# Optimization experiments

Hardware: AMD Instinct MI355X
Metric: run time of the kernel (lower is better)

Reference implementation:

```python
import jax, jax.numpy as jnp
import numpy as np

IN_CH = 512
MID_CH = IN_CH // 8  # 64


def setup_inputs() -> dict:
    key = jax.random.key(0)
    ks = jax.random.split(key, 7)
    B, C, H, W = 8, IN_CH, 64, 64
    s = 1.0 / np.sqrt(C)
    x = jax.random.normal(ks[0], (B, C, H, W), dtype=jnp.float32)
    wq = jax.random.normal(ks[1], (MID_CH, C), dtype=jnp.float32) * s
    bq = jax.random.normal(ks[2], (MID_CH,), dtype=jnp.float32) * 0.01
    wk = jax.random.normal(ks[3], (MID_CH, C), dtype=jnp.float32) * s
    bk = jax.random.normal(ks[4], (MID_CH,), dtype=jnp.float32) * 0.01
    wv = jax.random.normal(ks[5], (C, C), dtype=jnp.float32) * s
    bv = jax.random.normal(ks[6], (C,), dtype=jnp.float32) * 0.01
    gamma = jnp.array([0.5], dtype=jnp.float32)
    return {"x": x, "wq": wq, "bq": bq, "wk": wk, "bk": bk,
            "wv": wv, "bv": bv, "gamma": gamma}


def reference(x, wq, bq, wk, bk, wv, bv, gamma):
    B, C, H, W = x.shape
    N = H * W
    xf = x.reshape(B, C, N)  # flatten spatial -> [B, C, N]
    # 1x1 convs are channel-wise matmuls
    q = jnp.einsum('mc,bcn->bnm', wq, xf) + bq  # [B, N, mid]
    k = jnp.einsum('mc,bcn->bmn', wk, xf) + bk[None, :, None]  # [B, mid, N]
    v = jnp.einsum('oc,bcn->bon', wv, xf) + bv[None, :, None]  # [B, C, N]
    sim = jnp.einsum('bnm,bmj->bnj', q, k)  # [B, N, N]
    sim = jax.nn.softmax(sim, axis=-1)
    # feat[b,c,i] = sum_j v[b,c,j] * sim[b,i,j]   (value @ sim^T)
    feat = jnp.einsum('bcj,bij->bci', v, sim).reshape(B, C, H, W)
    return gamma[0] * feat + x
```

## Files before the change

kernel.cpp:

```cpp
#include <hip/hip_runtime.h>
#include <hip/hip_bf16.h>


#define BB 8
#define CC 512
#define MM 64
#define NN 4096
#define LOG2E 1.4426950408889634f

typedef __attribute__((ext_vector_type(8))) short bf16x8;
typedef __attribute__((ext_vector_type(8))) _Float16 f16x8;
typedef __attribute__((ext_vector_type(4))) float f32x4;

__device__ unsigned g_kmax[BB];

__device__ __forceinline__ unsigned short f2bf(float f) {
  union { float f; unsigned u; } v; v.f = f;
  unsigned r = v.u + 0x7fffu + ((v.u >> 16) & 1u);
  return (unsigned short)(r >> 16);
}
__device__ __forceinline__ float bf2f(unsigned short h) {
  union { unsigned u; float f; } v; v.u = ((unsigned)h) << 16;
  return v.f;
}
__device__ __forceinline__ unsigned short f2h(float f) {
  union { _Float16 h; unsigned short u; } v; v.h = (_Float16)f;
  return v.u;
}

__global__ __launch_bounds__(256) void k_wconv(
    const float* __restrict__ wq, const float* __restrict__ wk,
    const float* __restrict__ wv,
    unsigned short* __restrict__ wqhi, unsigned short* __restrict__ wqlo,
    unsigned short* __restrict__ wkhi, unsigned short* __restrict__ wklo,
    unsigned short* __restrict__ wvbf) {
  const int tid = blockIdx.x * 256 + threadIdx.x;
  if (tid < BB) g_kmax[tid] = 0u;
  if (tid < MM * CC) {
    float v = wq[tid];
    unsigned short h = f2bf(v);
    wqhi[tid] = h; wqlo[tid] = f2bf(v - bf2f(h));
    v = wk[tid]; h = f2bf(v);
    wkhi[tid] = h; wklo[tid] = f2bf(v - bf2f(h));
  }
  for (int i = tid; i < CC * CC; i += 65536) wvbf[i] = f2bf(wv[i]);
}

__global__ __launch_bounds__(256) void k_transpose(const float* __restrict__ x,
                                                   unsigned short* __restrict__ xT) {
  __shared__ float tile[64][65];
  const int b = blockIdx.z, c0 = blockIdx.y * 64, n0 = blockIdx.x * 64;
  const int t = threadIdx.x;
  {
    const int nl = t & 63, cl0 = t >> 6;
    const float* xp = x + ((size_t)b * CC + c0) * NN + n0;
#pragma unroll
    for (int r = 0; r < 16; r++) {
      const int cl = cl0 + r * 4;
      tile[cl][nl] = xp[(size_t)cl * NN + nl];
    }
  }
  __syncthreads();
  {
    const int cl = t & 63, nl0 = t >> 6;
    unsigned short* xtp = xT + ((size_t)b * NN + n0) * CC + c0;
#pragma unroll
    for (int r = 0; r < 16; r++) {
      const int nl = nl0 + r * 4;
      xtp[(size_t)nl * CC + cl] = f2bf(tile[cl][nl]);
    }
  }
}

__global__ __launch_bounds__(256, 2) void k_proj(
    const unsigned short* __restrict__ xT,
    const unsigned short* __restrict__ wqhi, const unsigned short* __restrict__ wqlo,
    const unsigned short* __restrict__ wkhi, const unsigned short* __restrict__ wklo,
    const float* __restrict__ bq, const float* __restrict__ bk,
    const unsigned short* __restrict__ wvbf, const float* __restrict__ bv,
    unsigned short* __restrict__ qf, unsigned short* __restrict__ kf,
    unsigned short* __restrict__ vbf) {
  __shared__ float ksl[4][4][16];
  const int t = threadIdx.x, w = t >> 6, l = t & 63, lr = l & 15, g = l >> 4;

  if (blockIdx.x < 512) {
    const int b = blockIdx.x & 7;
    const int n0 = (blockIdx.x >> 3) * 64;
    const unsigned short* qhp = wqhi + (size_t)(w * 16 + lr) * CC + g * 8;
    const unsigned short* qlp = wqlo + (size_t)(w * 16 + lr) * CC + g * 8;
    const unsigned short* khp = wkhi + (size_t)(w * 16 + lr) * CC + g * 8;
    const unsigned short* klp = wklo + (size_t)(w * 16 + lr) * CC + g * 8;
    const unsigned short* xp = xT + ((size_t)b * NN + n0 + lr) * CC + g * 8;
    f32x4 qacc[4], kacc[4];
#pragma unroll
    for (int nf = 0; nf < 4; nf++) {
      qacc[nf] = f32x4{0.f, 0.f, 0.f, 0.f};
      kacc[nf] = f32x4{0.f, 0.f, 0.f, 0.f};
    }
    for (int cc = 0; cc < CC; cc += 32) {
      const bf16x8 qh8 = *reinterpret_cast<const bf16x8*>(qhp + cc);
      const bf16x8 ql8 = *reinterpret_cast<const bf16x8*>(qlp + cc);
      const bf16x8 kh8 = *reinterpret_cast<const bf16x8*>(khp + cc);
      const bf16x8 kl8 = *reinterpret_cast<const bf16x8*>(klp + cc);
      bf16x8 xb[4];
#pragma unroll
      for (int nf = 0; nf < 4; nf++)
        xb[nf] = *reinterpret_cast<const bf16x8*>(xp + (size_t)nf * 16 * CC + cc);
#pragma unroll
      for (int nf = 0; nf < 4; nf++) {
        qacc[nf] = __builtin_amdgcn_mfma_f32_16x16x32_bf16(qh8, xb[nf], qacc[nf], 0, 0, 0);
        qacc[nf] = __builtin_amdgcn_mfma_f32_16x16x32_bf16(ql8, xb[nf], qacc[nf], 0, 0, 0);
        kacc[nf] = __builtin_amdgcn_mfma_f32_16x16x32_bf16(kh8, xb[nf], kacc[nf], 0, 0, 0);
        kacc[nf] = __builtin_amdgcn_mfma_f32_16x16x32_bf16(kl8, xb[nf], kacc[nf], 0, 0, 0);
      }
    }
    float bqv[4], bkv[4];
#pragma unroll
    for (int r = 0; r < 4; r++) {
      bqv[r] = bq[w * 16 + g * 4 + r];
      bkv[r] = bk[w * 16 + g * 4 + r];
    }
    float kssp[4];
#pragma unroll
    for (int nf = 0; nf < 4; nf++) {
      float ks2 = 0.f;
      unsigned short qh[4], kh[4];
#pragma unroll
      for (int r = 0; r < 4; r++) {
        const float qv = (qacc[nf][r] + bqv[r]) * LOG2E;
        const float kv = kacc[nf][r] + bkv[r];
        qh[r] = f2h(qv); kh[r] = f2h(kv);
        ks2 += kv * kv;
      }
      kssp[nf] = ks2;
      const int n = n0 + nf * 16 + lr;
      const size_t base = ((size_t)b * NN + n) * MM + w * 16 + g * 4;
      *reinterpret_cast<ushort4*>(qf + base) = make_ushort4(qh[0], qh[1], qh[2], qh[3]);
      *reinterpret_cast<ushort4*>(kf + base) = make_ushort4(kh[0], kh[1], kh[2], kh[3]);
    }
#pragma unroll
    for (int nf = 0; nf < 4; nf++) {
      kssp[nf] += __shfl_xor(kssp[nf], 16);
      kssp[nf] += __shfl_xor(kssp[nf], 32);
    }
    if (l < 16) {
#pragma unroll
      for (int nf = 0; nf < 4; nf++) ksl[w][nf][lr] = kssp[nf];
    }
    __syncthreads();
    if (t < 64) {
      const int nf2 = t >> 4, lr2 = t & 15;
      float kn2 = ksl[0][nf2][lr2] + ksl[1][nf2][lr2] + ksl[2][nf2][lr2] + ksl[3][nf2][lr2];
#pragma unroll
      for (int d = 1; d < 64; d <<= 1) kn2 = fmaxf(kn2, __shfl_xor(kn2, d));
      if (t == 0) atomicMax(&g_kmax[b], __float_as_uint(kn2));
    }
  } else {
    const int blk = blockIdx.x - 512;
    const int b = blk >> 8, c0 = ((blk >> 5) & 7) * 64, n0 = (blk & 31) * 128;
    const int nbase = n0 + w * 32;
    f32x4 acc[4][2];
#pragma unroll
    for (int cf = 0; cf < 4; cf++) {
      acc[cf][0] = f32x4{0.f, 0.f, 0.f, 0.f};
      acc[cf][1] = f32x4{0.f, 0.f, 0.f, 0.f};
    }
    for (int ks = 0; ks < 16; ks++) {
      const int kk = ks * 32 + g * 8;
      bf16x8 bfr[2];
#pragma unroll
      for (int nf = 0; nf < 2; nf++) {
        const int n = nbase + nf * 16 + lr;
        bfr[nf] = *reinterpret_cast<const bf16x8*>(xT + ((size_t)b * NN + n) * CC + kk);
      }
#pragma unroll
      for (int cf = 0; cf < 4; cf++) {
        const bf16x8 af = *reinterpret_cast<const bf16x8*>(
            wvbf + (size_t)(c0 + cf * 16 + lr) * CC + kk);
        acc[cf][0] = __builtin_amdgcn_mfma_f32_16x16x32_bf16(af, bfr[0], acc[cf][0], 0, 0, 0);
        acc[cf][1] = __builtin_amdgcn_mfma_f32_16x16x32_bf16(af, bfr[1], acc[cf][1], 0, 0, 0);
      }
    }
#pragma unroll
    for (int cf = 0; cf < 4; cf++) {
#pragma unroll
      for (int r = 0; r < 4; r++) {
        const int c = c0 + cf * 16 + g * 4 + r;
        const float bvv = bv[c];
#pragma unroll
        for (int nf = 0; nf < 2; nf++) {
          const int n = nbase + nf * 16 + lr;
          vbf[((size_t)b * CC + c) * NN + n] = f2bf(acc[cf][nf][r] + bvv);
        }
      }
    }
  }
}

__global__ __launch_bounds__(512, 2) void k_attn(
    const unsigned short* __restrict__ qf, const unsigned short* __restrict__ kf,
    const unsigned short* __restrict__ vbf, const float* __restrict__ x,
    const float* __restrict__ gamma, float* __restrict__ out) {
  __shared__ unsigned short P_lds[2][128][64];
  __shared__ float l_red[8][4][16];
  const int b = blockIdx.x & 7;
  const int idx = blockIdx.x >> 3;
  const int i0 = (idx >> 1) * 128;
  const int ch = idx & 1;
  const int t = threadIdx.x, w = t >> 6, l = t & 63, lr = l & 15, g = l >> 4;
  const int jf = w & 3, ig = w >> 2;
  const int wc = ch * 256 + w * 32;

  f16x8 qF[4][2];
#pragma unroll
  for (int q = 0; q < 4; q++) {
    const int i = i0 + (ig * 4 + q) * 16 + lr;
#pragma unroll
    for (int ks = 0; ks < 2; ks++)
      qF[q][ks] = *reinterpret_cast<const f16x8*>(qf + ((size_t)b * NN + i) * MM + ks * 32 + g * 8);
  }
  float mhat[4];
  {
    const float kroot = sqrtf(__uint_as_float(g_kmax[b])) * 1.001f;
#pragma unroll
    for (int q = 0; q < 4; q++) {
      float ssq = 0.f;
#pragma unroll
      for (int ks = 0; ks < 2; ks++)
#pragma unroll
        for (int e = 0; e < 8; e++) {
          const float qv = (float)qF[q][ks][e];
          ssq += qv * qv;
        }
      ssq += __shfl_xor(ssq, 16);
      ssq += __shfl_xor(ssq, 32);
      mhat[q] = sqrtf(ssq) * kroot - 63.4786f;
    }
  }

  const unsigned short* kp = kf + ((size_t)b * NN + jf * 16 + lr) * MM + g * 8;
  const unsigned short* pv = vbf + ((size_t)b * CC + wc + lr) * NN + g * 8;

  f32x4 acc[2][8];
#pragma unroll
  for (int cf = 0; cf < 2; cf++)
#pragma unroll
    for (int i2 = 0; i2 < 8; i2++) acc[cf][i2] = f32x4{0.f, 0.f, 0.f, 0.f};
  float lsum[4] = {0.f, 0.f, 0.f, 0.f};

  char* const pbase = (char*)&P_lds[0][0][0];
  int off_s[4];
#pragma unroll
  for (int q = 0; q < 4; q++) {
    const int row = (ig * 4 + q) * 16 + lr;
    off_s[q] = (row << 7) + ((jf * 32 + g * 8) ^ ((row & 7) << 4));
  }

  f16x8 kA[2], kB[2];
#pragma unroll
  for (int ks = 0; ks < 2; ks++)
    kA[ks] = *reinterpret_cast<const f16x8*>(kp + (size_t)ks * 32);
  bf16x8 va[2][2], vb[2][2];
#pragma unroll
  for (int ks = 0; ks < 2; ks++)
#pragma unroll
    for (int cf = 0; cf < 2; cf++)
      va[ks][cf] = *reinterpret_cast<const bf16x8*>(pv + (size_t)cf * (16 * NN) + ks * 32);
#pragma unroll
  for (int q = 0; q < 4; q++) {
    f32x4 sa = __builtin_amdgcn_mfma_f32_16x16x32_f16(kA[0], qF[q][0],
                                                      f32x4{0.f, 0.f, 0.f, 0.f}, 0, 0, 0);
    sa = __builtin_amdgcn_mfma_f32_16x16x32_f16(kA[1], qF[q][1], sa, 0, 0, 0);
    const float p0 = __builtin_amdgcn_exp2f(sa[0] - mhat[q]);
    const float p1 = __builtin_amdgcn_exp2f(sa[1] - mhat[q]);
    const float p2 = __builtin_amdgcn_exp2f(sa[2] - mhat[q]);
    const float p3 = __builtin_amdgcn_exp2f(sa[3] - mhat[q]);
    lsum[q] += (p0 + p1) + (p2 + p3);
    unsigned r01, r23;
    asm volatile("v_cvt_pk_bf16_f32 %0, %1, %2" : "=v"(r01) : "v"(p0), "v"(p1));
    asm volatile("v_cvt_pk_bf16_f32 %0, %1, %2" : "=v"(r23) : "v"(p2), "v"(p3));
    *reinterpret_cast<uint2*>(pbase + off_s[q]) = make_uint2(r01, r23);
  }
#pragma unroll
  for (int ks = 0; ks < 2; ks++)
    kB[ks] = *reinterpret_cast<const f16x8*>(kp + (size_t)64 * MM + ks * 32);
  __builtin_amdgcn_sched_barrier(0);
  asm volatile("s_waitcnt lgkmcnt(0)" ::: "memory");
  __builtin_amdgcn_s_barrier();
  __builtin_amdgcn_sched_barrier(0);

  auto region = [&](int jb, bf16x8 (&vcur)[2][2], bf16x8 (&vnext)[2][2],
                    f16x8 (&kuse)[2], f16x8 (&kpre)[2]) {
    const int par = (jb >> 6) & 1;
    const int j1 = (jb + 64) & (NN - 1);
    const int j2 = (jb + 128) & (NN - 1);
#pragma unroll
    for (int ks = 0; ks < 2; ks++)
#pragma unroll
      for (int cf = 0; cf < 2; cf++)
        vnext[ks][cf] = *reinterpret_cast<const bf16x8*>(
            pv + (size_t)cf * (16 * NN) + j1 + ks * 32);
    f32x4 sa[4];
#pragma unroll
    for (int q = 0; q < 4; q++) {
      sa[q] = __builtin_amdgcn_mfma_f32_16x16x32_f16(kuse[0], qF[q][0],
                                                     f32x4{0.f, 0.f, 0.f, 0.f}, 0, 0, 0);
      sa[q] = __builtin_amdgcn_mfma_f32_16x16x32_f16(kuse[1], qF[q][1], sa[q], 0, 0, 0);
    }
#pragma unroll
    for (int ks = 0; ks < 2; ks++)
      kpre[ks] = *reinterpret_cast<const f16x8*>(kp + (size_t)j2 * MM + ks * 32);
    const bool vld = (jb + 64) < NN;
    char* const pw = pbase + ((par ^ 1) << 14);
#pragma unroll
    for (int q = 0; q < 4; q++) {
      const float p0 = __builtin_amdgcn_exp2f(sa[q][0] - mhat[q]);
      const float p1 = __builtin_amdgcn_exp2f(sa[q][1] - mhat[q]);
      const float p2 = __builtin_amdgcn_exp2f(sa[q][2] - mhat[q]);
      const float p3 = __builtin_amdgcn_exp2f(sa[q][3] - mhat[q]);
      if (vld) lsum[q] += (p0 + p1) + (p2 + p3);
      unsigned r01, r23;
      asm volatile("v_cvt_pk_bf16_f32 %0, %1, %2" : "=v"(r01) : "v"(p0), "v"(p1));
      asm volatile("v_cvt_pk_bf16_f32 %0, %1, %2" : "=v"(r23) : "v"(p2), "v"(p3));
      *reinterpret_cast<uint2*>(pw + off_s[q]) = make_uint2(r01, r23);
    }
    char* const pr = pbase + (par << 14);
    __builtin_amdgcn_s_setprio(1);
#pragma unroll
    for (int ks = 0; ks < 2; ks++) {
#pragma unroll
      for (int i2 = 0; i2 < 8; i2++) {
        const int row = i2 * 16 + lr;
        const int colb = ks * 64 + g * 16;
        const bf16x8 pf = *reinterpret_cast<const bf16x8*>(
            pr + (row << 7) + (colb ^ ((row & 7) << 4)));
        acc[0][i2] = __builtin_amdgcn_mfma_f32_16x16x32_bf16(vcur[ks][0], pf, acc[0][i2], 0, 0, 0);
        acc[1][i2] = __builtin_amdgcn_mfma_f32_16x16x32_bf16(vcur[ks][1], pf, acc[1][i2], 0, 0, 0);
      }
    }
    __builtin_amdgcn_s_setprio(0);
    __builtin_amdgcn_sched_barrier(0);
    asm volatile("s_waitcnt lgkmcnt(0)" ::: "memory");
    __builtin_amdgcn_s_barrier();
    __builtin_amdgcn_sched_barrier(0);
  };

  for (int tt = 0; tt < 32; tt++) {
    region(tt * 128, va, vb, kB, kA);
    region(tt * 128 + 64, vb, va, kA, kB);
  }

#pragma unroll
  for (int q = 0; q < 4; q++) {
    lsum[q] += __shfl_xor(lsum[q], 16);
    lsum[q] += __shfl_xor(lsum[q], 32);
  }
  __syncthreads();
  if (l < 16) {
#pragma unroll
    for (int q = 0; q < 4; q++) l_red[w][q][lr] = lsum[q];
  }
  __syncthreads();
  const float gm = gamma[0];
  float inv[8];
#pragma unroll
  for (int i2 = 0; i2 < 8; i2++) {
    const int ig2 = i2 >> 2, q = i2 & 3;
    inv[i2] = gm / (l_red[ig2 * 4 + 0][q][lr] + l_red[ig2 * 4 + 1][q][lr] +
                    l_red[ig2 * 4 + 2][q][lr] + l_red[ig2 * 4 + 3][q][lr]);
  }

#pragma unroll
  for (int cf = 0; cf < 2; cf++) {
#pragma unroll
    for (int r = 0; r < 4; r++) {
      const int c = wc + cf * 16 + g * 4 + r;
      const size_t rowo = ((size_t)b * CC + c) * NN;
#pragma unroll
      for (int i2 = 0; i2 < 8; i2++) {
        const int i = i0 + i2 * 16 + lr;
        out[rowo + i] = acc[cf][i2][r] * inv[i2] + x[rowo + i];
      }
    }
  }
}

extern "C" void kernel_launch(void* const* d_in, const int* in_sizes, int n_in,
                              void* d_out, int out_size, void* d_ws, size_t ws_size,
                              hipStream_t stream) {
  const float* x = (const float*)d_in[0];
  const float* wq = (const float*)d_in[1];
  const float* bq = (const float*)d_in[2];
  const float* wk = (const float*)d_in[3];
  const float* bk = (const float*)d_in[4];
  const float* wv = (const float*)d_in[5];
  const float* bv = (const float*)d_in[6];
  const float* gamma = (const float*)d_in[7];
  float* out = (float*)d_out;

  char* ws = (char*)d_ws;
  unsigned short* xT = (unsigned short*)(ws);
  unsigned short* vbf = (unsigned short*)(ws + 33554432);
  unsigned short* qfp = (unsigned short*)(ws + 67108864);
  unsigned short* kfp = (unsigned short*)(ws + 71303168);
  unsigned short* wqhi = (unsigned short*)(ws + 75497472);
  unsigned short* wqlo = (unsigned short*)(ws + 75563008);
  unsigned short* wkhi = (unsigned short*)(ws + 75628544);
  unsigned short* wklo = (unsigned short*)(ws + 75694080);
  unsigned short* wvbf = (unsigned short*)(ws + 75759616);

  k_wconv<<<256, 256, 0, stream>>>(wq, wk, wv, wqhi, wqlo, wkhi, wklo, wvbf);
  k_transpose<<<dim3(64, 8, 8), 256, 0, stream>>>(x, xT);
  k_proj<<<2560, 256, 0, stream>>>(xT, wqhi, wqlo, wkhi, wklo, bq, bk, wvbf, bv,
                                   qfp, kfp, vbf);
  k_attn<<<dim3(512), 512, 0, stream>>>(qfp, kfp, vbf, x, gamma, out);
}
```

Before: 335.6 us.

## Retile attention to 256-thread blocks, widen V-proj tiles, vectorize transpose

Attention blocks shrink to 256 threads covering 64 query rows by 256 channels, so each wave owns 64 channels over 4 query fragments. V fragments are now loaded per region instead of prefetched a region ahead, and the PV MFMAs are moved ahead of the exp/softmax writes. The V projection doubles its per-wave N tile to reduce the block count, and the transpose uses float4 loads and ushort4 stores. Together these change occupancy, register pressure and the overlap between loads and compute, and dropping the V prefetch risks exposing global load latency.

```diff
diff --git a/kernel.cpp b/kernel.cpp
--- a/kernel.cpp
+++ b/kernel.cpp
@@ -52,22 +52,26 @@
   const int b = blockIdx.z, c0 = blockIdx.y * 64, n0 = blockIdx.x * 64;
   const int t = threadIdx.x;
   {
-    const int nl = t & 63, cl0 = t >> 6;
+    const int nq = (t & 15) * 4, cl0 = t >> 4;
     const float* xp = x + ((size_t)b * CC + c0) * NN + n0;
 #pragma unroll
-    for (int r = 0; r < 16; r++) {
-      const int cl = cl0 + r * 4;
-      tile[cl][nl] = xp[(size_t)cl * NN + nl];
+    for (int r = 0; r < 4; r++) {
+      const int row = cl0 + r * 16;
+      const f32x4 v = *reinterpret_cast<const f32x4*>(xp + (size_t)row * NN + nq);
+      tile[row][nq] = v[0]; tile[row][nq + 1] = v[1];
+      tile[row][nq + 2] = v[2]; tile[row][nq + 3] = v[3];
     }
   }
   __syncthreads();
   {
-    const int cl = t & 63, nl0 = t >> 6;
+    const int cq = (t & 15) * 4, nl0 = t >> 4;
     unsigned short* xtp = xT + ((size_t)b * NN + n0) * CC + c0;
 #pragma unroll
-    for (int r = 0; r < 16; r++) {
-      const int nl = nl0 + r * 4;
-      xtp[(size_t)nl * CC + cl] = f2bf(tile[cl][nl]);
+    for (int r = 0; r < 4; r++) {
+      const int n = nl0 + r * 16;
+      const ushort4 o = make_ushort4(f2bf(tile[cq][n]), f2bf(tile[cq + 1][n]),
+                                     f2bf(tile[cq + 2][n]), f2bf(tile[cq + 3][n]));
+      *reinterpret_cast<ushort4*>(xtp + (size_t)n * CC + cq) = o;
     }
   }
 }
@@ -157,19 +161,18 @@
     }
   } else {
     const int blk = blockIdx.x - 512;
-    const int b = blk >> 8, c0 = ((blk >> 5) & 7) * 64, n0 = (blk & 31) * 128;
-    const int nbase = n0 + w * 32;
-    f32x4 acc[4][2];
-#pragma unroll
-    for (int cf = 0; cf < 4; cf++) {
-      acc[cf][0] = f32x4{0.f, 0.f, 0.f, 0.f};
-      acc[cf][1] = f32x4{0.f, 0.f, 0.f, 0.f};
-    }
+    const int b = blk >> 7, c0 = ((blk >> 4) & 7) * 64, n0 = (blk & 15) * 256;
+    const int nbase = n0 + w * 64;
+    f32x4 acc[4][4];
+#pragma unroll
+    for (int cf = 0; cf < 4; cf++)
+#pragma unroll
+      for (int nf = 0; nf < 4; nf++) acc[cf][nf] = f32x4{0.f, 0.f, 0.f, 0.f};
     for (int ks = 0; ks < 16; ks++) {
       const int kk = ks * 32 + g * 8;
-      bf16x8 bfr[2];
-#pragma unroll
-      for (int nf = 0; nf < 2; nf++) {
+      bf16x8 bfr[4];
+#pragma unroll
+      for (int nf = 0; nf < 4; nf++) {
         const int n = nbase + nf * 16 + lr;
         bfr[nf] = *reinterpret_cast<const bf16x8*>(xT + ((size_t)b * NN + n) * CC + kk);
       }
@@ -177,8 +180,9 @@
       for (int cf = 0; cf < 4; cf++) {
         const bf16x8 af = *reinterpret_cast<const bf16x8*>(
             wvbf + (size_t)(c0 + cf * 16 + lr) * CC + kk);
-        acc[cf][0] = __builtin_amdgcn_mfma_f32_16x16x32_bf16(af, bfr[0], acc[cf][0], 0, 0, 0);
-        acc[cf][1] = __builtin_amdgcn_mfma_f32_16x16x32_bf16(af, bfr[1], acc[cf][1], 0, 0, 0);
+#pragma unroll
+        for (int nf = 0; nf < 4; nf++)
+          acc[cf][nf] = __builtin_amdgcn_mfma_f32_16x16x32_bf16(af, bfr[nf], acc[cf][nf], 0, 0, 0);
       }
     }
 #pragma unroll
@@ -188,7 +192,7 @@
         const int c = c0 + cf * 16 + g * 4 + r;
         const float bvv = bv[c];
 #pragma unroll
-        for (int nf = 0; nf < 2; nf++) {
+        for (int nf = 0; nf < 4; nf++) {
           const int n = nbase + nf * 16 + lr;
           vbf[((size_t)b * CC + c) * NN + n] = f2bf(acc[cf][nf][r] + bvv);
         }
@@ -197,24 +201,24 @@
   }
 }
 
-__global__ __launch_bounds__(512, 2) void k_attn(
+__global__ __launch_bounds__(256, 2) void k_attn(
     const unsigned short* __restrict__ qf, const unsigned short* __restrict__ kf,
     const unsigned short* __restrict__ vbf, const float* __restrict__ x,
     const float* __restrict__ gamma, float* __restrict__ out) {
-  __shared__ unsigned short P_lds[2][128][64];
-  __shared__ float l_red[8][4][16];
+  __shared__ unsigned short P_lds[2][64][64];
+  __shared__ float l_red[4][4][16];
   const int b = blockIdx.x & 7;
   const int idx = blockIdx.x >> 3;
-  const int i0 = (idx >> 1) * 128;
+  const int i0 = (idx >> 1) * 64;
   const int ch = idx & 1;
   const int t = threadIdx.x, w = t >> 6, l = t & 63, lr = l & 15, g = l >> 4;
-  const int jf = w & 3, ig = w >> 2;
-  const int wc = ch * 256 + w * 32;
+  const int jf = w;
+  const int wc = ch * 256 + w * 64;
 
   f16x8 qF[4][2];
 #pragma unroll
   for (int q = 0; q < 4; q++) {
-    const int i = i0 + (ig * 4 + q) * 16 + lr;
+    const int i = i0 + q * 16 + lr;
 #pragma unroll
     for (int ks = 0; ks < 2; ks++)
       qF[q][ks] = *reinterpret_cast<const f16x8*>(qf + ((size_t)b * NN + i) * MM + ks * 32 + g * 8);
@@ -241,18 +245,19 @@
   const unsigned short* kp = kf + ((size_t)b * NN + jf * 16 + lr) * MM + g * 8;
   const unsigned short* pv = vbf + ((size_t)b * CC + wc + lr) * NN + g * 8;
 
-  f32x4 acc[2][8];
-#pragma unroll
-  for (int cf = 0; cf < 2; cf++)
-#pragma unroll
-    for (int i2 = 0; i2 < 8; i2++) acc[cf][i2] = f32x4{0.f, 0.f, 0.f, 0.f};
+  f32x4 acc[4][4];
+#pragma unroll
+  for (int cf = 0; cf < 4; cf++)
+#pragma unroll
+    for (int i2 = 0; i2 < 4; i2++) acc[cf][i2] = f32x4{0.f, 0.f, 0.f, 0.f};
   float lsum[4] = {0.f, 0.f, 0.f, 0.f};
 
   char* const pbase = (char*)&P_lds[0][0][0];
+  const int rswz = (lr & 7) << 4;
   int off_s[4];
 #pragma unroll
   for (int q = 0; q < 4; q++) {
-    const int row = (ig * 4 + q) * 16 + lr;
+    const int row = q * 16 + lr;
     off_s[q] = (row << 7) + ((jf * 32 + g * 8) ^ ((row & 7) << 4));
   }
 
@@ -260,12 +265,6 @@
 #pragma unroll
   for (int ks = 0; ks < 2; ks++)
     kA[ks] = *reinterpret_cast<const f16x8*>(kp + (size_t)ks * 32);
-  bf16x8 va[2][2], vb[2][2];
-#pragma unroll
-  for (int ks = 0; ks < 2; ks++)
-#pragma unroll
-    for (int cf = 0; cf < 2; cf++)
-      va[ks][cf] = *reinterpret_cast<const bf16x8*>(pv + (size_t)cf * (16 * NN) + ks * 32);
 #pragma unroll
   for (int q = 0; q < 4; q++) {
     f32x4 sa = __builtin_amdgcn_mfma_f32_16x16x32_f16(kA[0], qF[q][0],
@@ -289,17 +288,16 @@
   __builtin_amdgcn_s_barrier();
   __builtin_amdgcn_sched_barrier(0);
 
-  auto region = [&](int jb, bf16x8 (&vcur)[2][2], bf16x8 (&vnext)[2][2],
-                    f16x8 (&kuse)[2], f16x8 (&kpre)[2]) {
+  auto region = [&](int jb, f16x8 (&kuse)[2], f16x8 (&kpre)[2]) {
     const int par = (jb >> 6) & 1;
-    const int j1 = (jb + 64) & (NN - 1);
     const int j2 = (jb + 128) & (NN - 1);
+    bf16x8 vr[2][4];
 #pragma unroll
     for (int ks = 0; ks < 2; ks++)
 #pragma unroll
-      for (int cf = 0; cf < 2; cf++)
-        vnext[ks][cf] = *reinterpret_cast<const bf16x8*>(
-            pv + (size_t)cf * (16 * NN) + j1 + ks * 32);
+      for (int cf = 0; cf < 4; cf++)
+        vr[ks][cf] = *reinterpret_cast<const bf16x8*>(
+            pv + (size_t)cf * (16 * NN) + jb + ks * 32);
     f32x4 sa[4];
 #pragma unroll
     for (int q = 0; q < 4; q++) {
@@ -310,8 +308,23 @@
 #pragma unroll
     for (int ks = 0; ks < 2; ks++)
       kpre[ks] = *reinterpret_cast<const f16x8*>(kp + (size_t)j2 * MM + ks * 32);
+    char* const pr = pbase + (par << 13);
+    __builtin_amdgcn_s_setprio(1);
+#pragma unroll
+    for (int ks = 0; ks < 2; ks++) {
+#pragma unroll
+      for (int i2 = 0; i2 < 4; i2++) {
+        const int row = i2 * 16 + lr;
+        const bf16x8 pf = *reinterpret_cast<const bf16x8*>(
+            pr + (row << 7) + ((ks * 64 + g * 16) ^ rswz));
+#pragma unroll
+        for (int cf = 0; cf < 4; cf++)
+          acc[cf][i2] = __builtin_amdgcn_mfma_f32_16x16x32_bf16(vr[ks][cf], pf, acc[cf][i2], 0, 0, 0);
+      }
+    }
+    __builtin_amdgcn_s_setprio(0);
     const bool vld = (jb + 64) < NN;
-    char* const pw = pbase + ((par ^ 1) << 14);
+    char* const pw = pbase + ((par ^ 1) << 13);
 #pragma unroll
     for (int q = 0; q < 4; q++) {
       const float p0 = __builtin_amdgcn_exp2f(sa[q][0] - mhat[q]);
@@ -324,21 +337,6 @@
       asm volatile("v_cvt_pk_bf16_f32 %0, %1, %2" : "=v"(r23) : "v"(p2), "v"(p3));
       *reinterpret_cast<uint2*>(pw + off_s[q]) = make_uint2(r01, r23);
     }
-    char* const pr = pbase + (par << 14);
-    __builtin_amdgcn_s_setprio(1);
-#pragma unroll
-    for (int ks = 0; ks < 2; ks++) {
-#pragma unroll
-      for (int i2 = 0; i2 < 8; i2++) {
-        const int row = i2 * 16 + lr;
-        const int colb = ks * 64 + g * 16;
-        const bf16x8 pf = *reinterpret_cast<const bf16x8*>(
-            pr + (row << 7) + (colb ^ ((row & 7) << 4)));
-        acc[0][i2] = __builtin_amdgcn_mfma_f32_16x16x32_bf16(vcur[ks][0], pf, acc[0][i2], 0, 0, 0);
-        acc[1][i2] = __builtin_amdgcn_mfma_f32_16x16x32_bf16(vcur[ks][1], pf, acc[1][i2], 0, 0, 0);
-      }
-    }
-    __builtin_amdgcn_s_setprio(0);
     __builtin_amdgcn_sched_barrier(0);
     asm volatile("s_waitcnt lgkmcnt(0)" ::: "memory");
     __builtin_amdgcn_s_barrier();
@@ -346,8 +344,8 @@
   };
 
   for (int tt = 0; tt < 32; tt++) {
-    region(tt * 128, va, vb, kB, kA);
-    region(tt * 128 + 64, vb, va, kA, kB);
+    region(tt * 128, kB, kA);
+    region(tt * 128 + 64, kA, kB);
   }
 
 #pragma unroll
@@ -355,29 +353,26 @@
     lsum[q] += __shfl_xor(lsum[q], 16);
     lsum[q] += __shfl_xor(lsum[q], 32);
   }
-  __syncthreads();
   if (l < 16) {
 #pragma unroll
     for (int q = 0; q < 4; q++) l_red[w][q][lr] = lsum[q];
   }
   __syncthreads();
   const float gm = gamma[0];
-  float inv[8];
-#pragma unroll
-  for (int i2 = 0; i2 < 8; i2++) {
-    const int ig2 = i2 >> 2, q = i2 & 3;
-    inv[i2] = gm / (l_red[ig2 * 4 + 0][q][lr] + l_red[ig2 * 4 + 1][q][lr] +
-                    l_red[ig2 * 4 + 2][q][lr] + l_red[ig2 * 4 + 3][q][lr]);
-  }
-
-#pragma unroll
-  for (int cf = 0; cf < 2; cf++) {
+  float inv[4];
+#pragma unroll
+  for (int i2 = 0; i2 < 4; i2++)
+    inv[i2] = gm / (l_red[0][i2][lr] + l_red[1][i2][lr] +
+                    l_red[2][i2][lr] + l_red[3][i2][lr]);
+
+#pragma unroll
+  for (int cf = 0; cf < 4; cf++) {
 #pragma unroll
     for (int r = 0; r < 4; r++) {
       const int c = wc + cf * 16 + g * 4 + r;
       const size_t rowo = ((size_t)b * CC + c) * NN;
 #pragma unroll
-      for (int i2 = 0; i2 < 8; i2++) {
+      for (int i2 = 0; i2 < 4; i2++) {
         const int i = i0 + i2 * 16 + lr;
         out[rowo + i] = acc[cf][i2][r] * inv[i2] + x[rowo + i];
       }
@@ -411,7 +406,7 @@
 
   k_wconv<<<256, 256, 0, stream>>>(wq, wk, wv, wqhi, wqlo, wkhi, wklo, wvbf);
   k_transpose<<<dim3(64, 8, 8), 256, 0, stream>>>(x, xT);
-  k_proj<<<2560, 256, 0, stream>>>(xT, wqhi, wqlo, wkhi, wklo, bq, bk, wvbf, bv,
+  k_proj<<<1536, 256, 0, stream>>>(xT, wqhi, wqlo, wkhi, wklo, bq, bk, wvbf, bv,
                                    qfp, kfp, vbf);
-  k_attn<<<dim3(512), 512, 0, stream>>>(qfp, kfp, vbf, x, gamma, out);
-}
+  k_attn<<<dim3(1024), 256, 0, stream>>>(qfp, kfp, vbf, x, gamma, out);
+}
```

Result: slower. 416.8 us (+24.2%).
